# Performance work log

Hardware: AMD Instinct MI355X
Metric: run time of the kernel (lower is better)

The kernel has to match this reference:

```python
import jax, jax.numpy as jnp
import numpy as np

D_MODEL = 1024
NUM_HEADS = 16
D_K = D_MODEL // NUM_HEADS
THETA = 10000.0
MAX_SEQ_LEN = 4096


def setup_inputs() -> dict:
    key = jax.random.key(0)
    ks = jax.random.split(key, 5)
    scale = 1.0 / np.sqrt(D_MODEL)
    x = jax.random.normal(ks[0], (2, 2048, D_MODEL), dtype=jnp.float32)
    wq = jax.random.normal(ks[1], (D_MODEL, D_MODEL), dtype=jnp.float32) * scale
    wk = jax.random.normal(ks[2], (D_MODEL, D_MODEL), dtype=jnp.float32) * scale
    wv = jax.random.normal(ks[3], (D_MODEL, D_MODEL), dtype=jnp.float32) * scale
    wo = jax.random.normal(ks[4], (D_MODEL, D_MODEL), dtype=jnp.float32) * scale
    return {"x": x, "wq": wq, "wk": wk, "wv": wv, "wo": wo}


def _rope(t, cos, sin):
    # t: (B, H, S, d_k) with interleaved even/odd pairs
    pairs = t.reshape(*t.shape[:-1], D_K // 2, 2)
    e, o = pairs[..., 0], pairs[..., 1]
    oe = e * cos - o * sin
    oo = e * sin + o * cos
    return jnp.stack([oe, oo], axis=-1).reshape(t.shape)


def reference(x, wq, wk, wv, wo):
    B, S, _ = x.shape
    # QKV projections (Linear: y = x @ W^T, no bias)
    def proj(w):
        y = jnp.einsum('bsd,ed->bse', x, w)
        return y.reshape(B, S, NUM_HEADS, D_K).transpose(0, 2, 1, 3)  # (B,H,S,dk)
    q, k, v = proj(wq), proj(wk), proj(wv)

    # RoPE angles for positions 0..S-1
    pair_idx = jnp.arange(0, D_K, 2, dtype=jnp.float32)
    inv_freq = 1.0 / (THETA ** (pair_idx / D_K))
    pos = jnp.arange(S, dtype=jnp.float32)
    ang = pos[:, None] * inv_freq[None, :]          # (S, dk/2)
    cos, sin = jnp.cos(ang), jnp.sin(ang)
    q = _rope(q, cos, sin)
    k = _rope(k, cos, sin)

    scores = jnp.einsum('bhqd,bhkd->bhqk', q, k) / jnp.sqrt(jnp.float32(D_K))
    causal = jnp.tril(jnp.ones((S, S), dtype=bool))
    scores = jnp.where(causal, scores, jnp.finfo(scores.dtype).min)
    attn = jax.nn.softmax(scores, axis=-1)
    out = jnp.einsum('bhqk,bhkd->bhqd', attn, v)    # (B,H,S,dk)
    out = out.transpose(0, 2, 1, 3).reshape(B, S, D_MODEL)
    return jnp.einsum('bsd,ed->bse', out, wo)
```

## Files before the change

kernel.cpp:

```cpp
#include <hip/hip_runtime.h>
#include <hip/hip_bf16.h>
#include <stdint.h>

#define S_LEN  2048
#define DMODEL 1024
#define NHEADS 16
#define DKH    64
#define NBATCH 2
#define NROWS  (NBATCH * S_LEN)
#define NBH    (NBATCH * NHEADS)
#define KVS    72

typedef unsigned short ushort_t;
typedef __attribute__((ext_vector_type(8))) short bf16x8;
typedef __attribute__((ext_vector_type(4))) float f32x4;
typedef __attribute__((ext_vector_type(4))) unsigned short us4;
typedef __attribute__((ext_vector_type(4))) unsigned int u32x4;

__device__ __forceinline__ ushort_t f2bf(float f) {
  union { float f; unsigned int u; } c; c.f = f;
  unsigned int r = c.u + 0x7FFFu + ((c.u >> 16) & 1u);
  return (ushort_t)(r >> 16);
}

__device__ __forceinline__ unsigned int pack_bf16(float lo, float hi) {
  union { __hip_bfloat162 h; unsigned int u; } cv;
  cv.h = __float22bfloat162_rn(make_float2(lo, hi));
  return cv.u;
}

__device__ __forceinline__ void gload_lds16(const void* g, void* l) {
  __builtin_amdgcn_global_load_lds((const __attribute__((address_space(1))) void*)g,
                                   (__attribute__((address_space(3))) void*)l, 16, 0, 0);
}

__global__ void cast5_kernel(const float* __restrict__ x,
                             const float* __restrict__ a, const float* __restrict__ b,
                             const float* __restrict__ c, const float* __restrict__ d,
                             ushort_t* __restrict__ dst) {
  const int i = (blockIdx.x * 256 + threadIdx.x) * 4;
  const int sel = i >> 20;
  const float* src;
  int off;
  if (sel < 4)      { src = x; off = i; }
  else if (sel == 4){ src = a; off = i & ((1 << 20) - 1); }
  else if (sel == 5){ src = b; off = i & ((1 << 20) - 1); }
  else if (sel == 6){ src = c; off = i & ((1 << 20) - 1); }
  else              { src = d; off = i & ((1 << 20) - 1); }
  const float4 v = *(const float4*)(src + off);
  us4 o;
  o.x = f2bf(v.x); o.y = f2bf(v.y); o.z = f2bf(v.z); o.w = f2bf(v.w);
  *(us4*)(dst + i) = o;
}

template<int EPI>
__device__ __forceinline__ void gemm_core(const ushort_t* __restrict__ A, const ushort_t* __restrict__ Bm,
                                          void* __restrict__ Cp, void* __restrict__ Cp2,
                                          int N, int r0, int c0,
                                          ushort_t* As, ushort_t* Bs)
{
  const int tid  = threadIdx.x;
  const int lane = tid & 63;
  const int w    = tid >> 6;
  const int wr   = (w >> 1) * 64;
  const int wc   = (w & 1) * 64;
  const int g    = lane >> 4;
  const int lr   = lane & 15;
  const int K    = 1024;

  f32x4 acc[4][4] = {};

  const int idx0 = tid, idx1 = 256 + tid;
  const int row0 = idx0 >> 2, ce0 = (idx0 & 3) * 8;
  const int row1 = idx1 >> 2, ce1 = (idx1 & 3) * 8;

  for (int k0 = 0; k0 < K; k0 += 32) {
    gload_lds16(A  + (size_t)(r0 + row0) * K + k0 + ce0, As + idx0 * 8);
    gload_lds16(A  + (size_t)(r0 + row1) * K + k0 + ce1, As + idx1 * 8);
    gload_lds16(Bm + (size_t)(c0 + row0) * K + k0 + ce0, Bs + idx0 * 8);
    gload_lds16(Bm + (size_t)(c0 + row1) * K + k0 + ce1, Bs + idx1 * 8);
    __syncthreads();
    bf16x8 af[4], bfr[4];
    #pragma unroll
    for (int i = 0; i < 4; i++) {
      af[i]  = *(const bf16x8*)(As + (wr + i * 16 + lr) * 32 + g * 8);
      bfr[i] = *(const bf16x8*)(Bs + (wc + i * 16 + lr) * 32 + g * 8);
    }
    #pragma unroll
    for (int mf = 0; mf < 4; mf++)
      #pragma unroll
      for (int nf = 0; nf < 4; nf++)
        acc[mf][nf] = __builtin_amdgcn_mfma_f32_16x16x32_bf16(af[mf], bfr[nf], acc[mf][nf], 0, 0, 0);
    __syncthreads();
  }

  #pragma unroll
  for (int mf = 0; mf < 4; mf++) {
    #pragma unroll
    for (int nf = 0; nf < 4; nf++) {
      #pragma unroll
      for (int r = 0; r < 4; r++) {
        const int row = r0 + wr + mf * 16 + g * 4 + r;
        const int col = c0 + wc + nf * 16 + lr;
        float v = acc[mf][nf][r];
        if constexpr (EPI == 0) {
          ((ushort_t*)Cp)[(size_t)row * N + col] = f2bf(v);
        } else {
          float pv = __shfl_xor(v, 1);
          const int cc  = col & (DMODEL - 1);
          const int pos = row & (S_LEN - 1);
          const int d   = cc & (DKH - 1);
          const int pr  = d >> 1;
          const float inv = exp2f((float)pr * -0.41524100952f);
          const float ang = (float)pos * inv;
          float sn, cs;
          __sincosf(ang, &sn, &cs);
          float outv = (d & 1) ? (pv * sn + v * cs) : (v * cs - pv * sn);
          if (col < DMODEL) outv *= 0.125f;
          const int b = row >> 11, s = row & (S_LEN - 1);
          const int h = cc >> 6;
          ushort_t* dst = (ushort_t*)((col < DMODEL) ? Cp : Cp2);
          dst[(((size_t)(b * NHEADS + h)) * S_LEN + s) * DKH + d] = f2bf(outv);
        }
      }
    }
  }
}

__global__ __launch_bounds__(256, 2)
void proj_kernel(const ushort_t* __restrict__ xb, const ushort_t* __restrict__ wqb,
                 const ushort_t* __restrict__ wvb,
                 ushort_t* __restrict__ qb, ushort_t* __restrict__ kb, ushort_t* __restrict__ vtb)
{
  __shared__ ushort_t As[128 * 32];
  __shared__ ushort_t Bs[128 * 32];
  const int lin = (int)blockIdx.x;
  const int nl  = (lin & 7) * 96 + (lin >> 3);
  if (nl < 512) {
    gemm_core<2>(xb, wqb, qb, kb, 2 * DMODEL, (nl >> 4) * 128, (nl & 15) * 128, As, Bs);
  } else {
    const int m = nl - 512;
    gemm_core<0>(wvb, xb, vtb, nullptr, NROWS, (m >> 5) * 128, (m & 31) * 128, As, Bs);
  }
}

__global__ __launch_bounds__(256, 2)
void gemm_final(const ushort_t* __restrict__ A, const ushort_t* __restrict__ Bm,
                float* __restrict__ Cp)
{
  __shared__ ushort_t As[128 * 32];
  __shared__ ushort_t Bs[128 * 32];
  const int gx   = 8;
  const int lin  = (int)blockIdx.y * gx + (int)blockIdx.x;
  const int nl   = (lin & 7) * 32 + (lin >> 3);
  const int r0   = (nl / gx) * 128;
  const int c0   = (nl % gx) * 128;
  const int tid  = threadIdx.x;
  const int lane = tid & 63;
  const int w    = tid >> 6;
  const int wr   = (w >> 1) * 64;
  const int wc   = (w & 1) * 64;
  const int g    = lane >> 4;
  const int lr   = lane & 15;
  const int K    = 1024;

  f32x4 acc[4][4] = {};
  const int idx0 = tid, idx1 = 256 + tid;
  const int row0 = idx0 >> 2, ce0 = (idx0 & 3) * 8;
  const int row1 = idx1 >> 2, ce1 = (idx1 & 3) * 8;

  for (int k0 = 0; k0 < K; k0 += 32) {
    gload_lds16(A  + (size_t)(r0 + row0) * K + k0 + ce0, As + idx0 * 8);
    gload_lds16(A  + (size_t)(r0 + row1) * K + k0 + ce1, As + idx1 * 8);
    gload_lds16(Bm + (size_t)(c0 + row0) * K + k0 + ce0, Bs + idx0 * 8);
    gload_lds16(Bm + (size_t)(c0 + row1) * K + k0 + ce1, Bs + idx1 * 8);
    __syncthreads();
    bf16x8 af[4], bfr[4];
    #pragma unroll
    for (int i = 0; i < 4; i++) {
      af[i]  = *(const bf16x8*)(As + (wr + i * 16 + lr) * 32 + g * 8);
      bfr[i] = *(const bf16x8*)(Bs + (wc + i * 16 + lr) * 32 + g * 8);
    }
    #pragma unroll
    for (int mf = 0; mf < 4; mf++)
      #pragma unroll
      for (int nf = 0; nf < 4; nf++)
        acc[mf][nf] = __builtin_amdgcn_mfma_f32_16x16x32_bf16(af[mf], bfr[nf], acc[mf][nf], 0, 0, 0);
    __syncthreads();
  }
  #pragma unroll
  for (int mf = 0; mf < 4; mf++)
    #pragma unroll
    for (int nf = 0; nf < 4; nf++)
      #pragma unroll
      for (int r = 0; r < 4; r++) {
        const int row = r0 + wr + mf * 16 + g * 4 + r;
        const int col = c0 + wc + nf * 16 + lr;
        Cp[(size_t)row * DMODEL + col] = acc[mf][nf][r];
      }
}

__global__ __launch_bounds__(512, 4)
void attn_kernel(const ushort_t* __restrict__ Q, const ushort_t* __restrict__ Kh,
                 const ushort_t* __restrict__ VT, ushort_t* __restrict__ Out)
{
  __shared__ ushort_t Ks[2][64 * KVS];
  __shared__ ushort_t Vs[2][64 * KVS];
  const int tid  = threadIdx.x;
  const int lane = tid & 63;
  const int w    = tid >> 6;
  const int grp  = w >> 2;
  const int wid  = w & 3;
  const int g    = lane >> 4, lr = lane & 15;

  const int id = (int)blockIdx.x;
  const int bh = id & 31;
  const int u  = (id >> 5) & 7;
  const int j  = id >> 8;
  const int qt = (j == 0) ? u : (j == 1) ? (15 - u) : (j == 2) ? (16 + u) : (31 - u);
  const int b  = bh >> 4, h = bh & 15;

  const ushort_t* Kbase = Kh + (size_t)bh * S_LEN * DKH;
  const ushort_t* Vbase = VT + (size_t)h * DKH * (size_t)NROWS + (size_t)b * S_LEN;

  ushort_t* Ksg = &Ks[grp][0];
  ushort_t* Vsg = &Vs[grp][0];
  float* MB = (float*)&Ks[1][0];
  float* SB = MB + 64 * 68;

  const int tg   = tid & 255;
  const int krow = tg >> 3;
  const int kcol = (tg & 7) * 8;

  const int qrow = qt * 64 + wid * 16;

  bf16x8 qf0, qf1;
  {
    const ushort_t* qp = Q + ((size_t)bh * S_LEN + qrow + lr) * DKH;
    qf0 = *(const bf16x8*)(qp + g * 8);
    qf1 = *(const bf16x8*)(qp + 32 + g * 8);
  }
  f32x4 o[4] = {};
  float lsum = 0.f;

  bf16x8 kr0, kr1, vr0, vr1;
  if (grp <= qt) {
    const int kv0 = grp * 64;
    kr0 = *(const bf16x8*)(Kbase + (size_t)(kv0 + krow) * DKH + kcol);
    kr1 = *(const bf16x8*)(Kbase + (size_t)(kv0 + 32 + krow) * DKH + kcol);
    vr0 = *(const bf16x8*)(Vbase + (size_t)krow * NROWS + kv0 + kcol);
    vr1 = *(const bf16x8*)(Vbase + (size_t)(32 + krow) * NROWS + kv0 + kcol);
  }

  const int nT = qt / 2 + 1;
  for (int t = 0; t < nT; t++) {
    const int tk  = 2 * t + grp;
    const bool act = (tk <= qt);
    const bool pre = (tk + 2 <= qt);

    __syncthreads();
    if (act) {
      *(bf16x8*)(Ksg + krow * KVS + kcol) = kr0;
      *(bf16x8*)(Ksg + (32 + krow) * KVS + kcol) = kr1;
      *(bf16x8*)(Vsg + krow * KVS + kcol) = vr0;
      *(bf16x8*)(Vsg + (32 + krow) * KVS + kcol) = vr1;
    }
    __syncthreads();
    if (pre) {
      const int kv0n = (tk + 2) * 64;
      kr0 = *(const bf16x8*)(Kbase + (size_t)(kv0n + krow) * DKH + kcol);
      kr1 = *(const bf16x8*)(Kbase + (size_t)(kv0n + 32 + krow) * DKH + kcol);
      vr0 = *(const bf16x8*)(Vbase + (size_t)krow * NROWS + kv0n + kcol);
      vr1 = *(const bf16x8*)(Vbase + (size_t)(32 + krow) * NROWS + kv0n + kcol);
    }

    if (act) {
      f32x4 s4[4];
      __builtin_amdgcn_s_setprio(1);
      #pragma unroll
      for (int nf = 0; nf < 4; nf++) {
        bf16x8 b0 = *(const bf16x8*)(Ksg + (nf * 16 + lr) * KVS + g * 8);
        bf16x8 b1 = *(const bf16x8*)(Ksg + (nf * 16 + lr) * KVS + 32 + g * 8);
        f32x4 z = {};
        z = __builtin_amdgcn_mfma_f32_16x16x32_bf16(b0, qf0, z, 0, 0, 0);
        z = __builtin_amdgcn_mfma_f32_16x16x32_bf16(b1, qf1, z, 0, 0, 0);
        s4[nf] = z;
      }
      __builtin_amdgcn_s_setprio(0);

      if (tk == qt) {
        const int qg = qrow + lr;
        #pragma unroll
        for (int nf = 0; nf < 4; nf++) {
          const int kvb = tk * 64 + nf * 16 + g * 4;
          #pragma unroll
          for (int r = 0; r < 4; r++)
            if (kvb + r > qg) s4[nf][r] = -3.0e38f;
        }
      }

      float p[4][4];
      #pragma unroll
      for (int nf = 0; nf < 4; nf++)
        #pragma unroll
        for (int r = 0; r < 4; r++) p[nf][r] = __expf(s4[nf][r]);
      lsum += ((p[0][0] + p[0][1]) + (p[0][2] + p[0][3])) + ((p[1][0] + p[1][1]) + (p[1][2] + p[1][3]))
            + ((p[2][0] + p[2][1]) + (p[2][2] + p[2][3])) + ((p[3][0] + p[3][1]) + (p[3][2] + p[3][3]));

      bf16x8 pa[2];
      const int src0 = ((g & 1) << 5) + lr;
      const int src1 = src0 + 16;
      const bool xl = (g < 2);
      #pragma unroll
      for (int kf = 0; kf < 2; kf++) {
        const unsigned int x0 = pack_bf16(p[2 * kf][0], p[2 * kf][1]);
        const unsigned int x1 = pack_bf16(p[2 * kf][2], p[2 * kf][3]);
        const unsigned int y0 = pack_bf16(p[2 * kf + 1][0], p[2 * kf + 1][1]);
        const unsigned int y1 = pack_bf16(p[2 * kf + 1][2], p[2 * kf + 1][3]);
        const unsigned int a0 = (unsigned int)__shfl((int)x0, src0);
        const unsigned int b0 = (unsigned int)__shfl((int)y0, src0);
        const unsigned int a1 = (unsigned int)__shfl((int)x1, src0);
        const unsigned int b1 = (unsigned int)__shfl((int)y1, src0);
        const unsigned int a2 = (unsigned int)__shfl((int)x0, src1);
        const unsigned int b2 = (unsigned int)__shfl((int)y0, src1);
        const unsigned int a3 = (unsigned int)__shfl((int)x1, src1);
        const unsigned int b3 = (unsigned int)__shfl((int)y1, src1);
        u32x4 wds;
        wds.x = xl ? a0 : b0;
        wds.y = xl ? a1 : b1;
        wds.z = xl ? a2 : b2;
        wds.w = xl ? a3 : b3;
        pa[kf] = *(bf16x8*)&wds;
      }

      __builtin_amdgcn_s_setprio(1);
      #pragma unroll
      for (int kf = 0; kf < 2; kf++)
        #pragma unroll
        for (int nf = 0; nf < 4; nf++) {
          const bf16x8 vB = *(const bf16x8*)(Vsg + (nf * 16 + lr) * KVS + kf * 32 + g * 8);
          o[nf] = __builtin_amdgcn_mfma_f32_16x16x32_bf16(pa[kf], vB, o[nf], 0, 0, 0);
        }
      __builtin_amdgcn_s_setprio(0);
    }
  }

  lsum += __shfl_xor(lsum, 16);
  lsum += __shfl_xor(lsum, 32);

  __syncthreads();
  if (grp == 1) {
    #pragma unroll
    for (int nf = 0; nf < 4; nf++)
      #pragma unroll
      for (int r = 0; r < 4; r++)
        MB[(wid * 16 + g * 4 + r) * 68 + nf * 16 + lr] = o[nf][r];
    if (g == 0) SB[wid * 16 + lr] = lsum;
  }
  __syncthreads();
  if (grp == 0) {
    #pragma unroll
    for (int r = 0; r < 4; r++) {
      const int rl  = g * 4 + r;
      const int rho = wid * 16 + rl;
      const float lB = SB[rho];
      const float lA = __shfl(lsum, (lane & 48) | rl);
      const float inv = 1.0f / (lA + lB);
      const int s = qt * 64 + rho;
      #pragma unroll
      for (int nf = 0; nf < 4; nf++) {
        const float val = (o[nf][r] + MB[rho * 68 + nf * 16 + lr]) * inv;
        Out[((size_t)b * S_LEN + s) * DMODEL + h * DKH + nf * 16 + lr] = f2bf(val);
      }
    }
  }
}

extern "C" void kernel_launch(void* const* d_in, const int* in_sizes, int n_in,
                              void* d_out, int out_size, void* d_ws, size_t ws_size,
                              hipStream_t stream)
{
  const float* x  = (const float*)d_in[0];
  const float* wq = (const float*)d_in[1];
  const float* wk = (const float*)d_in[2];
  const float* wv = (const float*)d_in[3];
  const float* wo = (const float*)d_in[4];
  float* out = (float*)d_out;
  ushort_t* ws = (ushort_t*)d_ws;

  ushort_t* xb  = ws;
  ushort_t* wqb = xb  + (size_t)NROWS * DMODEL;
  ushort_t* wkb = wqb + (size_t)DMODEL * DMODEL;
  ushort_t* wvb = wkb + (size_t)DMODEL * DMODEL;
  ushort_t* wob = wvb + (size_t)DMODEL * DMODEL;
  ushort_t* qb  = wob + (size_t)DMODEL * DMODEL;
  ushort_t* kb  = qb  + (size_t)NROWS * DMODEL;
  ushort_t* vtb = kb  + (size_t)NROWS * DMODEL;
  ushort_t* ab  = xb;

  cast5_kernel<<<8192, 256, 0, stream>>>(x, wq, wk, wv, wo, ws);

  proj_kernel<<<768, 256, 0, stream>>>(xb, wqb, wvb, qb, kb, vtb);
  attn_kernel<<<1024, 512, 0, stream>>>(qb, kb, vtb, ab);
  gemm_final<<<dim3(8, 32), 256, 0, stream>>>(ab, wob, out);
}
```

Before: 114.2 us.

## Load K/V fragments directly from global memory, dropping LDS staging and barriers

```diff
diff --git a/kernel.cpp b/kernel.cpp
--- a/kernel.cpp
+++ b/kernel.cpp
@@ -9,7 +9,6 @@
 #define NBATCH 2
 #define NROWS  (NBATCH * S_LEN)
 #define NBH    (NBATCH * NHEADS)
-#define KVS    72
 
 typedef unsigned short ushort_t;
 typedef __attribute__((ext_vector_type(8))) short bf16x8;
@@ -204,8 +203,8 @@
 void attn_kernel(const ushort_t* __restrict__ Q, const ushort_t* __restrict__ Kh,
                  const ushort_t* __restrict__ VT, ushort_t* __restrict__ Out)
 {
-  __shared__ ushort_t Ks[2][64 * KVS];
-  __shared__ ushort_t Vs[2][64 * KVS];
+  __shared__ float MB[64 * 68 + 64];
+  float* SB = MB + 64 * 68;
   const int tid  = threadIdx.x;
   const int lane = tid & 63;
   const int w    = tid >> 6;
@@ -215,22 +214,13 @@
 
   const int id = (int)blockIdx.x;
   const int bh = id & 31;
-  const int u  = (id >> 5) & 7;
-  const int j  = id >> 8;
-  const int qt = (j == 0) ? u : (j == 1) ? (15 - u) : (j == 2) ? (16 + u) : (31 - u);
+  const int u  = (id >> 5) & 15;
+  const int j  = id >> 9;
+  const int qt = j ? (31 - u) : u;
   const int b  = bh >> 4, h = bh & 15;
 
   const ushort_t* Kbase = Kh + (size_t)bh * S_LEN * DKH;
   const ushort_t* Vbase = VT + (size_t)h * DKH * (size_t)NROWS + (size_t)b * S_LEN;
-
-  ushort_t* Ksg = &Ks[grp][0];
-  ushort_t* Vsg = &Vs[grp][0];
-  float* MB = (float*)&Ks[1][0];
-  float* SB = MB + 64 * 68;
-
-  const int tg   = tid & 255;
-  const int krow = tg >> 3;
-  const int kcol = (tg & 7) * 8;
 
   const int qrow = qt * 64 + wid * 16;
 
@@ -243,112 +233,93 @@
   f32x4 o[4] = {};
   float lsum = 0.f;
 
-  bf16x8 kr0, kr1, vr0, vr1;
-  if (grp <= qt) {
-    const int kv0 = grp * 64;
-    kr0 = *(const bf16x8*)(Kbase + (size_t)(kv0 + krow) * DKH + kcol);
-    kr1 = *(const bf16x8*)(Kbase + (size_t)(kv0 + 32 + krow) * DKH + kcol);
-    vr0 = *(const bf16x8*)(Vbase + (size_t)krow * NROWS + kv0 + kcol);
-    vr1 = *(const bf16x8*)(Vbase + (size_t)(32 + krow) * NROWS + kv0 + kcol);
-  }
-
-  const int nT = qt / 2 + 1;
-  for (int t = 0; t < nT; t++) {
-    const int tk  = 2 * t + grp;
-    const bool act = (tk <= qt);
-    const bool pre = (tk + 2 <= qt);
-
-    __syncthreads();
-    if (act) {
-      *(bf16x8*)(Ksg + krow * KVS + kcol) = kr0;
-      *(bf16x8*)(Ksg + (32 + krow) * KVS + kcol) = kr1;
-      *(bf16x8*)(Vsg + krow * KVS + kcol) = vr0;
-      *(bf16x8*)(Vsg + (32 + krow) * KVS + kcol) = vr1;
-    }
-    __syncthreads();
-    if (pre) {
-      const int kv0n = (tk + 2) * 64;
-      kr0 = *(const bf16x8*)(Kbase + (size_t)(kv0n + krow) * DKH + kcol);
-      kr1 = *(const bf16x8*)(Kbase + (size_t)(kv0n + 32 + krow) * DKH + kcol);
-      vr0 = *(const bf16x8*)(Vbase + (size_t)krow * NROWS + kv0n + kcol);
-      vr1 = *(const bf16x8*)(Vbase + (size_t)(32 + krow) * NROWS + kv0n + kcol);
-    }
-
-    if (act) {
-      f32x4 s4[4];
-      __builtin_amdgcn_s_setprio(1);
+  for (int tk = grp; tk <= qt; tk += 2) {
+    const int kv0 = tk * 64;
+    const ushort_t* Kt = Kbase + (size_t)kv0 * DKH;
+
+    bf16x8 kb0[4], kb1[4];
+    #pragma unroll
+    for (int nf = 0; nf < 4; nf++) {
+      const ushort_t* kp = Kt + (size_t)(nf * 16 + lr) * DKH + g * 8;
+      kb0[nf] = *(const bf16x8*)(kp);
+      kb1[nf] = *(const bf16x8*)(kp + 32);
+    }
+
+    f32x4 s4[4];
+    __builtin_amdgcn_s_setprio(1);
+    #pragma unroll
+    for (int nf = 0; nf < 4; nf++) {
+      f32x4 z = {};
+      z = __builtin_amdgcn_mfma_f32_16x16x32_bf16(kb0[nf], qf0, z, 0, 0, 0);
+      z = __builtin_amdgcn_mfma_f32_16x16x32_bf16(kb1[nf], qf1, z, 0, 0, 0);
+      s4[nf] = z;
+    }
+    __builtin_amdgcn_s_setprio(0);
+
+    bf16x8 vb[2][4];
+    #pragma unroll
+    for (int kf = 0; kf < 2; kf++)
+      #pragma unroll
+      for (int nf = 0; nf < 4; nf++)
+        vb[kf][nf] = *(const bf16x8*)(Vbase + (size_t)(nf * 16 + lr) * NROWS + kv0 + kf * 32 + g * 8);
+
+    if (tk == qt) {
+      const int qg = qrow + lr;
       #pragma unroll
       for (int nf = 0; nf < 4; nf++) {
-        bf16x8 b0 = *(const bf16x8*)(Ksg + (nf * 16 + lr) * KVS + g * 8);
-        bf16x8 b1 = *(const bf16x8*)(Ksg + (nf * 16 + lr) * KVS + 32 + g * 8);
-        f32x4 z = {};
-        z = __builtin_amdgcn_mfma_f32_16x16x32_bf16(b0, qf0, z, 0, 0, 0);
-        z = __builtin_amdgcn_mfma_f32_16x16x32_bf16(b1, qf1, z, 0, 0, 0);
-        s4[nf] = z;
+        const int kvb = kv0 + nf * 16 + g * 4;
+        #pragma unroll
+        for (int r = 0; r < 4; r++)
+          if (kvb + r > qg) s4[nf][r] = -3.0e38f;
       }
-      __builtin_amdgcn_s_setprio(0);
-
-      if (tk == qt) {
-        const int qg = qrow + lr;
-        #pragma unroll
-        for (int nf = 0; nf < 4; nf++) {
-          const int kvb = tk * 64 + nf * 16 + g * 4;
-          #pragma unroll
-          for (int r = 0; r < 4; r++)
-            if (kvb + r > qg) s4[nf][r] = -3.0e38f;
-        }
-      }
-
-      float p[4][4];
+    }
+
+    float p[4][4];
+    #pragma unroll
+    for (int nf = 0; nf < 4; nf++)
+      #pragma unroll
+      for (int r = 0; r < 4; r++) p[nf][r] = __expf(s4[nf][r]);
+    lsum += ((p[0][0] + p[0][1]) + (p[0][2] + p[0][3])) + ((p[1][0] + p[1][1]) + (p[1][2] + p[1][3]))
+          + ((p[2][0] + p[2][1]) + (p[2][2] + p[2][3])) + ((p[3][0] + p[3][1]) + (p[3][2] + p[3][3]));
+
+    bf16x8 pa[2];
+    const int src0 = ((g & 1) << 5) + lr;
+    const int src1 = src0 + 16;
+    const bool xl = (g < 2);
+    #pragma unroll
+    for (int kf = 0; kf < 2; kf++) {
+      const unsigned int x0 = pack_bf16(p[2 * kf][0], p[2 * kf][1]);
+      const unsigned int x1 = pack_bf16(p[2 * kf][2], p[2 * kf][3]);
+      const unsigned int y0 = pack_bf16(p[2 * kf + 1][0], p[2 * kf + 1][1]);
+      const unsigned int y1 = pack_bf16(p[2 * kf + 1][2], p[2 * kf + 1][3]);
+      const unsigned int a0 = (unsigned int)__shfl((int)x0, src0);
+      const unsigned int b0 = (unsigned int)__shfl((int)y0, src0);
+      const unsigned int a1 = (unsigned int)__shfl((int)x1, src0);
+      const unsigned int b1 = (unsigned int)__shfl((int)y1, src0);
+      const unsigned int a2 = (unsigned int)__shfl((int)x0, src1);
+      const unsigned int b2 = (unsigned int)__shfl((int)y0, src1);
+      const unsigned int a3 = (unsigned int)__shfl((int)x1, src1);
+      const unsigned int b3 = (unsigned int)__shfl((int)y1, src1);
+      u32x4 wds;
+      wds.x = xl ? a0 : b0;
+      wds.y = xl ? a1 : b1;
+      wds.z = xl ? a2 : b2;
+      wds.w = xl ? a3 : b3;
+      pa[kf] = *(bf16x8*)&wds;
+    }
+
+    __builtin_amdgcn_s_setprio(1);
+    #pragma unroll
+    for (int kf = 0; kf < 2; kf++)
       #pragma unroll
       for (int nf = 0; nf < 4; nf++)
-        #pragma unroll
-        for (int r = 0; r < 4; r++) p[nf][r] = __expf(s4[nf][r]);
-      lsum += ((p[0][0] + p[0][1]) + (p[0][2] + p[0][3])) + ((p[1][0] + p[1][1]) + (p[1][2] + p[1][3]))
-            + ((p[2][0] + p[2][1]) + (p[2][2] + p[2][3])) + ((p[3][0] + p[3][1]) + (p[3][2] + p[3][3]));
-
-      bf16x8 pa[2];
-      const int src0 = ((g & 1) << 5) + lr;
-      const int src1 = src0 + 16;
-      const bool xl = (g < 2);
-      #pragma unroll
-      for (int kf = 0; kf < 2; kf++) {
-        const unsigned int x0 = pack_bf16(p[2 * kf][0], p[2 * kf][1]);
-        const unsigned int x1 = pack_bf16(p[2 * kf][2], p[2 * kf][3]);
-        const unsigned int y0 = pack_bf16(p[2 * kf + 1][0], p[2 * kf + 1][1]);
-        const unsigned int y1 = pack_bf16(p[2 * kf + 1][2], p[2 * kf + 1][3]);
-        const unsigned int a0 = (unsigned int)__shfl((int)x0, src0);
-        const unsigned int b0 = (unsigned int)__shfl((int)y0, src0);
-        const unsigned int a1 = (unsigned int)__shfl((int)x1, src0);
-        const unsigned int b1 = (unsigned int)__shfl((int)y1, src0);
-        const unsigned int a2 = (unsigned int)__shfl((int)x0, src1);
-        const unsigned int b2 = (unsigned int)__shfl((int)y0, src1);
-        const unsigned int a3 = (unsigned int)__shfl((int)x1, src1);
-        const unsigned int b3 = (unsigned int)__shfl((int)y1, src1);
-        u32x4 wds;
-        wds.x = xl ? a0 : b0;
-        wds.y = xl ? a1 : b1;
-        wds.z = xl ? a2 : b2;
-        wds.w = xl ? a3 : b3;
-        pa[kf] = *(bf16x8*)&wds;
-      }
-
-      __builtin_amdgcn_s_setprio(1);
-      #pragma unroll
-      for (int kf = 0; kf < 2; kf++)
-        #pragma unroll
-        for (int nf = 0; nf < 4; nf++) {
-          const bf16x8 vB = *(const bf16x8*)(Vsg + (nf * 16 + lr) * KVS + kf * 32 + g * 8);
-          o[nf] = __builtin_amdgcn_mfma_f32_16x16x32_bf16(pa[kf], vB, o[nf], 0, 0, 0);
-        }
-      __builtin_amdgcn_s_setprio(0);
-    }
+        o[nf] = __builtin_amdgcn_mfma_f32_16x16x32_bf16(pa[kf], vb[kf][nf], o[nf], 0, 0, 0);
+    __builtin_amdgcn_s_setprio(0);
   }
 
   lsum += __shfl_xor(lsum, 16);
   lsum += __shfl_xor(lsum, 32);
 
-  __syncthreads();
   if (grp == 1) {
     #pragma unroll
     for (int nf = 0; nf < 4; nf++)
```

After: 189.2 us. 65.6% more time.
